# Optimization experiments

Hardware: AMD Instinct MI355X
Metric: run time of the kernel (lower is better)

Reference implementation:

```python
import jax, jax.numpy as jnp
import numpy as np

NUM_NODES = 10000  # fixed by input spec: edge_index values in [0, 10000)


def setup_inputs() -> dict:
    key = jax.random.key(0)
    k1, k2, k3 = jax.random.split(key, 3)
    N, E, D_IN, D_OUT = NUM_NODES, 320000, 256, 256
    x = jax.random.normal(k1, (N, D_IN), dtype=jnp.float32)
    edge_index = jax.random.randint(k2, (2, E), 0, N, dtype=jnp.int64)
    # ensure node N-1 appears so num_nodes == N as in the torch code
    edge_index = edge_index.at[0, 0].set(N - 1)
    # xavier_uniform for [D_IN, D_OUT]
    limit = float(np.sqrt(6.0 / (D_IN + D_OUT)))
    weight = jax.random.uniform(k3, (D_IN, D_OUT), dtype=jnp.float32,
                                minval=-limit, maxval=limit)
    return {"x": x, "edge_index": edge_index, "weight": weight}


def _normalize_adjacency(edge_index, num_nodes):
    src, dst = edge_index[0], edge_index[1]
    ones = jnp.ones(src.shape[0], dtype=jnp.float32)
    # symmetric binarized adjacency: adj[i,j] = adj[j,i] = 1 (set, not add)
    adj = jnp.zeros((num_nodes, num_nodes), dtype=jnp.float32)
    adj = adj.at[src, dst].max(ones)
    adj = adj.at[dst, src].max(ones)
    # one round of self-loops: adj += I
    adj = adj + jnp.eye(num_nodes, dtype=jnp.float32)
    deg = jnp.sum(adj, axis=1)                    # [N]
    dinv = 1.0 / jnp.sqrt(deg)                    # [N]
    # D^-1/2 A D^-1/2 via broadcasting (equivalent to diag mms)
    return adj * dinv[:, None] * dinv[None, :]


def reference(x, edge_index, weight):
    adj = _normalize_adjacency(edge_index, NUM_NODES)  # [N, N]
    h = adj @ x                                        # [N, D_IN]
    return h @ weight                                  # [N, D_OUT]
```

## Files before the change

kernel.cpp:

```cpp
#include <hip/hip_runtime.h>
#include <hip/hip_bf16.h>
#include <stdint.h>

#define N_NODES   10000
#define D_FEAT    256
#define E_EDGES   320000
#define ROW_WORDS 313
#define ROW_STRIDE 320
#define LIST_CAP  1024

#define NB    250
#define RPB   40
#define B_CAP 8192

typedef __attribute__((ext_vector_type(4))) float float4v;
typedef _Float16 half8  __attribute__((ext_vector_type(8)));
typedef _Float16 half4v __attribute__((ext_vector_type(4)));

__device__ __forceinline__ uint16_t f2bf(float f) {
    union { float f; uint32_t u; } v; v.f = f;
    uint32_t r = v.u + 0x7fffu + ((v.u >> 16) & 1u);
    return (uint16_t)(r >> 16);
}
__device__ __forceinline__ float lo16(uint32_t u) {
    union { uint32_t u; float f; } v; v.u = u << 16; return v.f;
}
__device__ __forceinline__ float hi16(uint32_t u) {
    union { uint32_t u; float f; } v; v.u = u & 0xffff0000u; return v.f;
}


__global__ void __launch_bounds__(1024)
fill_buckets(const int* __restrict__ ei, uint32_t* __restrict__ bucketbuf,
             uint32_t* __restrict__ cursors) {
    __shared__ uint32_t hist[NB];
    __shared__ uint32_t base_s[NB];
    int t = threadIdx.x;
    for (int b = t; b < NB; b += 1024) hist[b] = 0;
    __syncthreads();
    int e = blockIdx.x * 1024 + t;
    int b0 = -1, b1 = -1; uint32_t ent0 = 0, ent1 = 0, slot0 = 0, slot1 = 0;
    if (e < E_EDGES) {
        int s = ei[e], d = ei[E_EDGES + e];
        if ((uint32_t)s < N_NODES && (uint32_t)d < N_NODES) {
            b0 = s / RPB; ent0 = ((uint32_t)(s - b0 * RPB) << 14) | (uint32_t)d;
            b1 = d / RPB; ent1 = ((uint32_t)(d - b1 * RPB) << 14) | (uint32_t)s;
            slot0 = atomicAdd(&hist[b0], 1u);
            slot1 = atomicAdd(&hist[b1], 1u);
        }
    }
    __syncthreads();
    for (int b = t; b < NB; b += 1024)
        base_s[b] = hist[b] ? atomicAdd(&cursors[b], hist[b]) : 0u;
    __syncthreads();
    if (b0 >= 0) {
        uint32_t p0 = base_s[b0] + slot0;
        if (p0 < B_CAP) bucketbuf[(size_t)b0 * B_CAP + p0] = ent0;
        uint32_t p1 = base_s[b1] + slot1;
        if (p1 < B_CAP) bucketbuf[(size_t)b1 * B_CAP + p1] = ent1;
    }
}

__global__ void __launch_bounds__(1024)
bucket_to_csr(const uint32_t* __restrict__ bucketbuf,
              const uint32_t* __restrict__ cursors,
              uint32_t* __restrict__ gcursor,
              uint32_t* __restrict__ col, uint32_t* __restrict__ row_base,
              uint32_t* __restrict__ row_deg, float* __restrict__ dinv) {
    __shared__ uint32_t bm[RPB * ROW_WORDS];
    __shared__ uint32_t degs[RPB];
    __shared__ uint32_t rowoff[RPB];
    __shared__ uint32_t segbase;
    int b = blockIdx.x, t = threadIdx.x;
    for (int i = t; i < RPB * ROW_WORDS; i += 1024) bm[i] = 0;
    __syncthreads();
    uint32_t cnt = min(cursors[b], (uint32_t)B_CAP);
    const uint32_t* bb = bucketbuf + (size_t)b * B_CAP;
    for (uint32_t i = t; i < cnt; i += 1024) {
        uint32_t ent = bb[i];
        uint32_t lr = ent >> 14, d = ent & 0x3FFFu;
        atomicOr(&bm[lr * ROW_WORDS + (d >> 5)], 1u << (d & 31));
    }
    __syncthreads();
    int wv = t >> 6, lane = t & 63;
    for (int r = wv; r < RPB; r += 16) {
        int pop = 0;
        #pragma unroll
        for (int k = 0; k < 5; k++) {
            int w = lane + 64 * k;
            if (w < ROW_WORDS) pop += __popc(bm[r * ROW_WORDS + w]);
        }
        #pragma unroll
        for (int off = 32; off > 0; off >>= 1) pop += __shfl_xor(pop, off, 64);
        if (lane == 0) degs[r] = (uint32_t)pop;
    }
    __syncthreads();
    if (t == 0) {
        uint32_t run = 0;
        for (int r = 0; r < RPB; r++) {
            rowoff[r] = run;
            run += (degs[r] + 3u) & ~3u;
        }
        segbase = atomicAdd(gcursor, run);
    }
    __syncthreads();
    int row0 = b * RPB;
    for (int r = wv; r < RPB; r += 16) {
        int gi = row0 + r;
        uint32_t base = segbase + rowoff[r];
        if (lane == 0) {
            row_base[gi] = base;
            row_deg[gi]  = degs[r];
            dinv[gi]     = 1.0f / sqrtf((float)(degs[r] + 1u));
        }
        uint32_t wb[5]; int tot = 0;
        #pragma unroll
        for (int k = 0; k < 5; k++) {
            int w = lane + 64 * k;
            uint32_t v = (w < ROW_WORDS) ? bm[r * ROW_WORDS + w] : 0u;
            wb[k] = v; tot += __popc(v);
        }
        int incl = tot;
        #pragma unroll
        for (int off = 1; off < 64; off <<= 1) {
            int v = __shfl_up(incl, off, 64);
            if (lane >= off) incl += v;
        }
        uint32_t p = base + (uint32_t)(incl - tot);
        #pragma unroll
        for (int k = 0; k < 5; k++) {
            uint32_t bits = wb[k];
            uint32_t cbase = (uint32_t)(lane + 64 * k) << 5;
            while (bits) {
                col[p++] = cbase + (uint32_t)__builtin_ctz(bits);
                bits &= bits - 1;
            }
        }
    }
}

__global__ void __launch_bounds__(256)
scale_cast(const float* __restrict__ dinv, const float* __restrict__ x,
           uint16_t* __restrict__ xs) {
    int wv = threadIdx.x >> 6, lane = threadIdx.x & 63;
    int i = blockIdx.x * 4 + wv;
    float di = dinv[i];
    float4v v = *(const float4v*)(x + (size_t)i * D_FEAT + lane * 4);
    uint2 o;
    o.x = (uint32_t)f2bf(di * v[0]) | ((uint32_t)f2bf(di * v[1]) << 16);
    o.y = (uint32_t)f2bf(di * v[2]) | ((uint32_t)f2bf(di * v[3]) << 16);
    *(uint2*)(xs + (size_t)i * D_FEAT + lane * 4) = o;
}

__global__ void __launch_bounds__(256)
wcast(const float* __restrict__ w, _Float16* __restrict__ wt) {
    int k = blockIdx.x, n = threadIdx.x;
    wt[(size_t)n * D_FEAT + k] = (_Float16)w[(size_t)k * D_FEAT + n];
}

__global__ void __launch_bounds__(256)
spmm_csr(const uint32_t* __restrict__ row_base, const uint32_t* __restrict__ row_deg,
         const float* __restrict__ dinv, const uint32_t* __restrict__ col,
         const uint16_t* __restrict__ xs, _Float16* __restrict__ aggh) {
    int wv = threadIdx.x >> 6, lane = threadIdx.x & 63;
    int i = blockIdx.x * 4 + wv;
    uint32_t base = row_base[i], deg = row_deg[i];
    float di = dinv[i];
    float4v z = {0.f, 0.f, 0.f, 0.f};
    float4v acc0 = z, acc1 = z, acc2 = z, acc3 = z;
    size_t ch = (size_t)lane * 4;
    uint32_t t4 = deg & ~3u;
    for (uint32_t t = 0; t < t4; t += 4) {
        uint4 jv = *(const uint4*)&col[base + t];
        uint2 g0 = *(const uint2*)(xs + (size_t)jv.x * D_FEAT + ch);
        uint2 g1 = *(const uint2*)(xs + (size_t)jv.y * D_FEAT + ch);
        uint2 g2 = *(const uint2*)(xs + (size_t)jv.z * D_FEAT + ch);
        uint2 g3 = *(const uint2*)(xs + (size_t)jv.w * D_FEAT + ch);
        acc0[0] += lo16(g0.x); acc0[1] += hi16(g0.x); acc0[2] += lo16(g0.y); acc0[3] += hi16(g0.y);
        acc1[0] += lo16(g1.x); acc1[1] += hi16(g1.x); acc1[2] += lo16(g1.y); acc1[3] += hi16(g1.y);
        acc2[0] += lo16(g2.x); acc2[1] += hi16(g2.x); acc2[2] += lo16(g2.y); acc2[3] += hi16(g2.y);
        acc3[0] += lo16(g3.x); acc3[1] += hi16(g3.x); acc3[2] += lo16(g3.y); acc3[3] += hi16(g3.y);
    }
    for (uint32_t t = t4; t < deg; t++) {
        uint32_t j = col[base + t];
        uint2 g = *(const uint2*)(xs + (size_t)j * D_FEAT + ch);
        acc0[0] += lo16(g.x); acc0[1] += hi16(g.x); acc0[2] += lo16(g.y); acc0[3] += hi16(g.y);
    }
    uint2 gs = *(const uint2*)(xs + (size_t)i * D_FEAT + ch);
    acc1[0] += lo16(gs.x); acc1[1] += hi16(gs.x); acc1[2] += lo16(gs.y); acc1[3] += hi16(gs.y);
    float4v acc = (acc0 + acc1) + (acc2 + acc3);
    half4v o = { (_Float16)(di * acc[0]), (_Float16)(di * acc[1]),
                 (_Float16)(di * acc[2]), (_Float16)(di * acc[3]) };
    *(half4v*)(aggh + (size_t)i * D_FEAT + ch) = o;
}

__global__ void __launch_bounds__(256)
gemm_mfma(const _Float16* __restrict__ aggh, const _Float16* __restrict__ wt,
          float* __restrict__ out) {
    int t = threadIdx.x;
    int wv = t >> 6, lane = t & 63;
    int quad = lane >> 4, r = lane & 15;
    int bx = blockIdx.x;
    int ct = blockIdx.y * 4 + wv;

    const _Float16* pa = aggh + (size_t)(bx * 16 + r) * D_FEAT + quad * 8;
    const _Float16* pb = wt   + (size_t)(ct * 16 + r) * D_FEAT + quad * 8;

    float4v acc = {0.f, 0.f, 0.f, 0.f};
    #pragma unroll
    for (int kk = 0; kk < D_FEAT; kk += 32) {
        half8 a = *(const half8*)(pa + kk);
        half8 b = *(const half8*)(pb + kk);
        acc = __builtin_amdgcn_mfma_f32_16x16x32_f16(a, b, acc, 0, 0, 0);
    }
    int mbase = bx * 16 + quad * 4;
    int colg  = ct * 16 + r;
    #pragma unroll
    for (int u = 0; u < 4; u++)
        out[(size_t)(mbase + u) * D_FEAT + colg] = acc[u];
}


__global__ void scatter_edges_fb(const int* __restrict__ ei,
                                 uint32_t* __restrict__ bitmap) {
    int e = blockIdx.x * blockDim.x + threadIdx.x;
    if (e >= E_EDGES) return;
    int s = ei[e], d = ei[E_EDGES + e];
    if ((uint32_t)s >= N_NODES || (uint32_t)d >= N_NODES) return;
    atomicOr(&bitmap[(size_t)s * ROW_STRIDE + (d >> 5)], 1u << (d & 31));
    atomicOr(&bitmap[(size_t)d * ROW_STRIDE + (s >> 5)], 1u << (s & 31));
}

__global__ void __launch_bounds__(256)
popc_dinv(const uint32_t* __restrict__ bitmap, float* __restrict__ dinv) {
    int wv = threadIdx.x >> 6, lane = threadIdx.x & 63;
    int i = blockIdx.x * 4 + wv;
    const uint32_t* rb = bitmap + (size_t)i * ROW_STRIDE;
    int pop = 0;
    #pragma unroll
    for (int k = 0; k < 5; k++) {
        int w = lane + 64 * k;
        if (w < ROW_WORDS) pop += __popc(rb[w]);
    }
    #pragma unroll
    for (int off = 32; off > 0; off >>= 1) pop += __shfl_xor(pop, off, 64);
    if (lane == 0) dinv[i] = 1.0f / sqrtf((float)(pop + 1));
}

__global__ void __launch_bounds__(256)
spmm_bitmap_fb(const uint32_t* __restrict__ bitmap, const float* __restrict__ dinv,
               const float* __restrict__ xf, float* __restrict__ agg) {
    __shared__ __align__(16) uint32_t lists[4][LIST_CAP];
    int wv = threadIdx.x >> 6, lane = threadIdx.x & 63;
    int i = blockIdx.x * 4 + wv;
    uint32_t* list = lists[wv];
    const uint32_t* rb = bitmap + (size_t)i * ROW_STRIDE;

    uint32_t wbits[5]; int tot = 0;
    #pragma unroll
    for (int k = 0; k < 5; k++) {
        int w = lane + 64 * k;
        uint32_t b = (w < ROW_WORDS) ? rb[w] : 0u;
        wbits[k] = b;
        tot += __popc(b);
    }
    int incl = tot;
    #pragma unroll
    for (int off = 1; off < 64; off <<= 1) {
        int v = __shfl_up(incl, off, 64);
        if (lane >= off) incl += v;
    }
    uint32_t p = (uint32_t)(incl - tot);
    uint32_t deg = (uint32_t)__shfl(incl, 63, 64);
    #pragma unroll
    for (int k = 0; k < 5; k++) {
        uint32_t bits = wbits[k];
        uint32_t base = (uint32_t)(lane + 64 * k) << 5;
        while (bits) {
            if (p < LIST_CAP) list[p] = base + (uint32_t)__builtin_ctz(bits);
            p++;
            bits &= bits - 1;
        }
    }
    if (deg > LIST_CAP) deg = LIST_CAP;

    float di = dinv[i];
    float4v z = {0.f, 0.f, 0.f, 0.f};
    float4v acc0 = z, acc1 = z, acc2 = z, acc3 = z;
    float4v sv = *(const float4v*)(xf + (size_t)i * D_FEAT + lane * 4);
    uint32_t t4 = deg & ~3u;
    for (uint32_t t = 0; t < t4; t += 4) {
        uint4 jv = *(const uint4*)&list[t];
        float d0 = dinv[jv.x], d1 = dinv[jv.y], d2 = dinv[jv.z], d3 = dinv[jv.w];
        float4v v0 = *(const float4v*)(xf + (size_t)jv.x * D_FEAT + lane * 4);
        float4v v1 = *(const float4v*)(xf + (size_t)jv.y * D_FEAT + lane * 4);
        float4v v2 = *(const float4v*)(xf + (size_t)jv.z * D_FEAT + lane * 4);
        float4v v3 = *(const float4v*)(xf + (size_t)jv.w * D_FEAT + lane * 4);
        acc0 += d0 * v0; acc1 += d1 * v1; acc2 += d2 * v2; acc3 += d3 * v3;
    }
    for (uint32_t t = t4; t < deg; t++) {
        uint32_t j = list[t];
        acc0 += dinv[j] * (*(const float4v*)(xf + (size_t)j * D_FEAT + lane * 4));
    }
    float4v acc = (acc0 + acc1) + (acc2 + acc3) + di * sv;
    *(float4v*)(agg + (size_t)i * D_FEAT + lane * 4) = di * acc;
}

__global__ void __launch_bounds__(256)
gemm_valu(float* __restrict__ io, const float* __restrict__ wf) {
    __shared__ __align__(16) float a_lds[16 * D_FEAT];
    int c = threadIdx.x;
    int r0 = blockIdx.x * 16;
    for (int idx = c; idx < 16 * D_FEAT; idx += 256)
        a_lds[idx] = io[(size_t)r0 * D_FEAT + idx];
    __syncthreads();
    float acc[16];
    #pragma unroll
    for (int r = 0; r < 16; r++) acc[r] = 0.f;
    for (int k0 = 0; k0 < D_FEAT; k0 += 4) {
        float w0 = wf[(size_t)(k0 + 0) * D_FEAT + c];
        float w1 = wf[(size_t)(k0 + 1) * D_FEAT + c];
        float w2 = wf[(size_t)(k0 + 2) * D_FEAT + c];
        float w3 = wf[(size_t)(k0 + 3) * D_FEAT + c];
        #pragma unroll
        for (int r = 0; r < 16; r++) {
            float4v av = *(const float4v*)&a_lds[r * D_FEAT + k0];
            acc[r] = fmaf(av[3], w3, fmaf(av[2], w2,
                     fmaf(av[1], w1, fmaf(av[0], w0, acc[r]))));
        }
    }
    #pragma unroll
    for (int r = 0; r < 16; r++)
        io[(size_t)(r0 + r) * D_FEAT + c] = acc[r];
}

extern "C" void kernel_launch(void* const* d_in, const int* in_sizes, int n_in,
                              void* d_out, int out_size, void* d_ws, size_t ws_size,
                              hipStream_t stream) {
    const float* x  = (const float*)d_in[0];
    const int*   ei = (const int*)d_in[1];
    const float* w  = (const float*)d_in[2];
    float* out = (float*)d_out;
    uint8_t* ws = (uint8_t*)d_ws;

    const size_t CUR_OFF  = 8192000;
    const size_t RB_OFF   = 8194048;
    const size_t RD_OFF   = 8234048;
    const size_t DI_OFF   = 8274048;
    const size_t XS_OFF   = 8314048;
    const size_t COL_OFF  = 13434048;
    const size_t WT_OFF   = 16154048;
    const size_t NEED_NEW = 16285120;
    const size_t NEED_FB  = 12840000;

    if (ws_size >= NEED_NEW) {
        uint32_t* bucketbuf = (uint32_t*)ws;
        _Float16* aggh      = (_Float16*)ws;
        uint32_t* cursors   = (uint32_t*)(ws + CUR_OFF);
        uint32_t* row_base  = (uint32_t*)(ws + RB_OFF);
        uint32_t* row_deg   = (uint32_t*)(ws + RD_OFF);
        float*    dinv      = (float*)(ws + DI_OFF);
        uint16_t* xs        = (uint16_t*)(ws + XS_OFF);
        uint32_t* col       = (uint32_t*)(ws + COL_OFF);
        _Float16* wt        = (_Float16*)(ws + WT_OFF);

        hipMemsetAsync(cursors, 0, 2048, stream);
        fill_buckets <<<(E_EDGES + 1023) / 1024, 1024, 0, stream>>>(ei, bucketbuf, cursors);
        bucket_to_csr<<<NB, 1024, 0, stream>>>(bucketbuf, cursors, &cursors[NB],
                                               col, row_base, row_deg, dinv);
        wcast        <<<D_FEAT, D_FEAT, 0, stream>>>(w, wt);
        scale_cast   <<<N_NODES / 4, 256, 0, stream>>>(dinv, x, xs);
        spmm_csr     <<<N_NODES / 4, 256, 0, stream>>>(row_base, row_deg, dinv, col, xs, aggh);
        gemm_mfma    <<<dim3(N_NODES / 16, 4), 256, 0, stream>>>(aggh, wt, out);
    } else if (ws_size >= NEED_FB) {
        uint32_t* bitmap = (uint32_t*)ws;
        float*    dinv   = (float*)(ws + 12800000);

        hipMemsetAsync(bitmap, 0, 12800000, stream);
        scatter_edges_fb<<<(E_EDGES + 255) / 256, 256, 0, stream>>>(ei, bitmap);
        popc_dinv      <<<N_NODES / 4, 256, 0, stream>>>(bitmap, dinv);
        spmm_bitmap_fb <<<N_NODES / 4, 256, 0, stream>>>(bitmap, dinv, x, out);
        gemm_valu      <<<N_NODES / 16, 256, 0, stream>>>(out, w);
    }
}
```

Baseline: 147.5 us.

## Fuse SpMM with MFMA GEMM via LDS and stage bucket writes in fill_buckets

Merges the sparse aggregation and the dense weight GEMM into one kernel. Each block aggregates 16 rows into LDS as fp16, then runs MFMA over all 256 output columns, so the intermediate aggregate never goes through global memory and one launch is removed. Separately, fill_buckets now does a local prefix scan and stages entries sorted by bucket in LDS, so the global bucket writes are more contiguous. The cost is fewer blocks for the SpMM (2500 down to 625), each doing 4 rows per wave, which lowers parallelism and latency hiding for the gather.

```diff
diff --git a/kernel.cpp b/kernel.cpp
--- a/kernel.cpp
+++ b/kernel.cpp
@@ -13,6 +13,8 @@
 #define RPB   40
 #define B_CAP 8192
 
+#define LDSTR 264
+
 typedef __attribute__((ext_vector_type(4))) float float4v;
 typedef _Float16 half8  __attribute__((ext_vector_type(8)));
 typedef _Float16 half4v __attribute__((ext_vector_type(4)));
@@ -33,31 +35,48 @@
 __global__ void __launch_bounds__(1024)
 fill_buckets(const int* __restrict__ ei, uint32_t* __restrict__ bucketbuf,
              uint32_t* __restrict__ cursors) {
-    __shared__ uint32_t hist[NB];
-    __shared__ uint32_t base_s[NB];
+    __shared__ uint32_t hist[256];
+    __shared__ uint32_t lofs[256];
+    __shared__ uint32_t base_s[256];
+    __shared__ uint32_t stage[2048];
+    __shared__ uint16_t sbkt[2048];
     int t = threadIdx.x;
-    for (int b = t; b < NB; b += 1024) hist[b] = 0;
+    if (t < 256) hist[t] = 0;
     __syncthreads();
     int e = blockIdx.x * 1024 + t;
-    int b0 = -1, b1 = -1; uint32_t ent0 = 0, ent1 = 0, slot0 = 0, slot1 = 0;
+    int b0 = -1, b1 = -1; uint32_t ent0 = 0, ent1 = 0, s0 = 0, s1 = 0;
     if (e < E_EDGES) {
         int s = ei[e], d = ei[E_EDGES + e];
         if ((uint32_t)s < N_NODES && (uint32_t)d < N_NODES) {
             b0 = s / RPB; ent0 = ((uint32_t)(s - b0 * RPB) << 14) | (uint32_t)d;
             b1 = d / RPB; ent1 = ((uint32_t)(d - b1 * RPB) << 14) | (uint32_t)s;
-            slot0 = atomicAdd(&hist[b0], 1u);
-            slot1 = atomicAdd(&hist[b1], 1u);
-        }
-    }
-    __syncthreads();
-    for (int b = t; b < NB; b += 1024)
-        base_s[b] = hist[b] ? atomicAdd(&cursors[b], hist[b]) : 0u;
-    __syncthreads();
+            s0 = atomicAdd(&hist[b0], 1u);
+            s1 = atomicAdd(&hist[b1], 1u);
+        }
+    }
+    __syncthreads();
+    if (t < 256) lofs[t] = hist[t];
+    __syncthreads();
+    for (int d = 1; d < 256; d <<= 1) {
+        uint32_t v = 0;
+        if (t < 256 && t >= d) v = lofs[t - d];
+        __syncthreads();
+        if (t < 256) lofs[t] += v;
+        __syncthreads();
+    }
+    if (t < 256) base_s[t] = hist[t] ? atomicAdd(&cursors[t], hist[t]) : 0u;
     if (b0 >= 0) {
-        uint32_t p0 = base_s[b0] + slot0;
-        if (p0 < B_CAP) bucketbuf[(size_t)b0 * B_CAP + p0] = ent0;
-        uint32_t p1 = base_s[b1] + slot1;
-        if (p1 < B_CAP) bucketbuf[(size_t)b1 * B_CAP + p1] = ent1;
+        uint32_t p0 = lofs[b0] - hist[b0] + s0;
+        stage[p0] = ent0; sbkt[p0] = (uint16_t)b0;
+        uint32_t p1 = lofs[b1] - hist[b1] + s1;
+        stage[p1] = ent1; sbkt[p1] = (uint16_t)b1;
+    }
+    __syncthreads();
+    uint32_t total = lofs[255];
+    for (uint32_t idx = t; idx < total; idx += 1024) {
+        uint32_t b = sbkt[idx];
+        uint32_t pos = base_s[b] + (idx - (lofs[b] - hist[b]));
+        if (pos < B_CAP) bucketbuf[(size_t)b * B_CAP + pos] = stage[idx];
     }
 }
 
@@ -159,65 +178,65 @@
 }
 
 __global__ void __launch_bounds__(256)
-spmm_csr(const uint32_t* __restrict__ row_base, const uint32_t* __restrict__ row_deg,
-         const float* __restrict__ dinv, const uint32_t* __restrict__ col,
-         const uint16_t* __restrict__ xs, _Float16* __restrict__ aggh) {
-    int wv = threadIdx.x >> 6, lane = threadIdx.x & 63;
-    int i = blockIdx.x * 4 + wv;
-    uint32_t base = row_base[i], deg = row_deg[i];
-    float di = dinv[i];
-    float4v z = {0.f, 0.f, 0.f, 0.f};
-    float4v acc0 = z, acc1 = z, acc2 = z, acc3 = z;
+spmm_gemm(const uint32_t* __restrict__ row_base, const uint32_t* __restrict__ row_deg,
+          const float* __restrict__ dinv, const uint32_t* __restrict__ col,
+          const uint16_t* __restrict__ xs, const _Float16* __restrict__ wt,
+          float* __restrict__ out) {
+    __shared__ __align__(16) _Float16 a_lds[16 * LDSTR];
+    int t = threadIdx.x, wv = t >> 6, lane = t & 63;
+    int r0 = blockIdx.x * 16;
     size_t ch = (size_t)lane * 4;
-    uint32_t t4 = deg & ~3u;
-    for (uint32_t t = 0; t < t4; t += 4) {
-        uint4 jv = *(const uint4*)&col[base + t];
-        uint2 g0 = *(const uint2*)(xs + (size_t)jv.x * D_FEAT + ch);
-        uint2 g1 = *(const uint2*)(xs + (size_t)jv.y * D_FEAT + ch);
-        uint2 g2 = *(const uint2*)(xs + (size_t)jv.z * D_FEAT + ch);
-        uint2 g3 = *(const uint2*)(xs + (size_t)jv.w * D_FEAT + ch);
-        acc0[0] += lo16(g0.x); acc0[1] += hi16(g0.x); acc0[2] += lo16(g0.y); acc0[3] += hi16(g0.y);
-        acc1[0] += lo16(g1.x); acc1[1] += hi16(g1.x); acc1[2] += lo16(g1.y); acc1[3] += hi16(g1.y);
-        acc2[0] += lo16(g2.x); acc2[1] += hi16(g2.x); acc2[2] += lo16(g2.y); acc2[3] += hi16(g2.y);
-        acc3[0] += lo16(g3.x); acc3[1] += hi16(g3.x); acc3[2] += lo16(g3.y); acc3[3] += hi16(g3.y);
-    }
-    for (uint32_t t = t4; t < deg; t++) {
-        uint32_t j = col[base + t];
-        uint2 g = *(const uint2*)(xs + (size_t)j * D_FEAT + ch);
-        acc0[0] += lo16(g.x); acc0[1] += hi16(g.x); acc0[2] += lo16(g.y); acc0[3] += hi16(g.y);
-    }
-    uint2 gs = *(const uint2*)(xs + (size_t)i * D_FEAT + ch);
-    acc1[0] += lo16(gs.x); acc1[1] += hi16(gs.x); acc1[2] += lo16(gs.y); acc1[3] += hi16(gs.y);
-    float4v acc = (acc0 + acc1) + (acc2 + acc3);
-    half4v o = { (_Float16)(di * acc[0]), (_Float16)(di * acc[1]),
-                 (_Float16)(di * acc[2]), (_Float16)(di * acc[3]) };
-    *(half4v*)(aggh + (size_t)i * D_FEAT + ch) = o;
-}
-
-__global__ void __launch_bounds__(256)
-gemm_mfma(const _Float16* __restrict__ aggh, const _Float16* __restrict__ wt,
-          float* __restrict__ out) {
-    int t = threadIdx.x;
-    int wv = t >> 6, lane = t & 63;
+
+    for (int rr = wv; rr < 16; rr += 4) {
+        int i = r0 + rr;
+        uint32_t base = row_base[i], deg = row_deg[i];
+        float di = dinv[i];
+        float4v z = {0.f, 0.f, 0.f, 0.f};
+        float4v acc0 = z, acc1 = z, acc2 = z, acc3 = z;
+        uint32_t t4 = deg & ~3u;
+        for (uint32_t k = 0; k < t4; k += 4) {
+            uint4 jv = *(const uint4*)&col[base + k];
+            uint2 g0 = *(const uint2*)(xs + (size_t)jv.x * D_FEAT + ch);
+            uint2 g1 = *(const uint2*)(xs + (size_t)jv.y * D_FEAT + ch);
+            uint2 g2 = *(const uint2*)(xs + (size_t)jv.z * D_FEAT + ch);
+            uint2 g3 = *(const uint2*)(xs + (size_t)jv.w * D_FEAT + ch);
+            acc0[0] += lo16(g0.x); acc0[1] += hi16(g0.x); acc0[2] += lo16(g0.y); acc0[3] += hi16(g0.y);
+            acc1[0] += lo16(g1.x); acc1[1] += hi16(g1.x); acc1[2] += lo16(g1.y); acc1[3] += hi16(g1.y);
+            acc2[0] += lo16(g2.x); acc2[1] += hi16(g2.x); acc2[2] += lo16(g2.y); acc2[3] += hi16(g2.y);
+            acc3[0] += lo16(g3.x); acc3[1] += hi16(g3.x); acc3[2] += lo16(g3.y); acc3[3] += hi16(g3.y);
+        }
+        for (uint32_t k = t4; k < deg; k++) {
+            uint32_t j = col[base + k];
+            uint2 g = *(const uint2*)(xs + (size_t)j * D_FEAT + ch);
+            acc0[0] += lo16(g.x); acc0[1] += hi16(g.x); acc0[2] += lo16(g.y); acc0[3] += hi16(g.y);
+        }
+        uint2 gs = *(const uint2*)(xs + (size_t)i * D_FEAT + ch);
+        acc1[0] += lo16(gs.x); acc1[1] += hi16(gs.x); acc1[2] += lo16(gs.y); acc1[3] += hi16(gs.y);
+        float4v acc = (acc0 + acc1) + (acc2 + acc3);
+        half4v o = { (_Float16)(di * acc[0]), (_Float16)(di * acc[1]),
+                     (_Float16)(di * acc[2]), (_Float16)(di * acc[3]) };
+        *(half4v*)&a_lds[rr * LDSTR + lane * 4] = o;
+    }
+    __syncthreads();
+
     int quad = lane >> 4, r = lane & 15;
-    int bx = blockIdx.x;
-    int ct = blockIdx.y * 4 + wv;
-
-    const _Float16* pa = aggh + (size_t)(bx * 16 + r) * D_FEAT + quad * 8;
-    const _Float16* pb = wt   + (size_t)(ct * 16 + r) * D_FEAT + quad * 8;
-
-    float4v acc = {0.f, 0.f, 0.f, 0.f};
-    #pragma unroll
-    for (int kk = 0; kk < D_FEAT; kk += 32) {
-        half8 a = *(const half8*)(pa + kk);
-        half8 b = *(const half8*)(pb + kk);
-        acc = __builtin_amdgcn_mfma_f32_16x16x32_f16(a, b, acc, 0, 0, 0);
-    }
-    int mbase = bx * 16 + quad * 4;
-    int colg  = ct * 16 + r;
-    #pragma unroll
-    for (int u = 0; u < 4; u++)
-        out[(size_t)(mbase + u) * D_FEAT + colg] = acc[u];
+    int mbase = r0 + quad * 4;
+    #pragma unroll
+    for (int u = 0; u < 4; u++) {
+        int ct = wv * 4 + u;
+        const _Float16* pb = wt + (size_t)(ct * 16 + r) * D_FEAT + quad * 8;
+        float4v acc = {0.f, 0.f, 0.f, 0.f};
+        #pragma unroll
+        for (int kk = 0; kk < D_FEAT; kk += 32) {
+            half8 a = *(const half8*)&a_lds[r * LDSTR + kk + quad * 8];
+            half8 b = *(const half8*)(pb + kk);
+            acc = __builtin_amdgcn_mfma_f32_16x16x32_f16(a, b, acc, 0, 0, 0);
+        }
+        int colg = ct * 16 + r;
+        #pragma unroll
+        for (int v = 0; v < 4; v++)
+            out[(size_t)(mbase + v) * D_FEAT + colg] = acc[v];
+    }
 }
 
 
@@ -289,8 +308,8 @@
     float4v acc0 = z, acc1 = z, acc2 = z, acc3 = z;
     float4v sv = *(const float4v*)(xf + (size_t)i * D_FEAT + lane * 4);
     uint32_t t4 = deg & ~3u;
-    for (uint32_t t = 0; t < t4; t += 4) {
-        uint4 jv = *(const uint4*)&list[t];
+    for (uint32_t k = 0; k < t4; k += 4) {
+        uint4 jv = *(const uint4*)&list[k];
         float d0 = dinv[jv.x], d1 = dinv[jv.y], d2 = dinv[jv.z], d3 = dinv[jv.w];
         float4v v0 = *(const float4v*)(xf + (size_t)jv.x * D_FEAT + lane * 4);
         float4v v1 = *(const float4v*)(xf + (size_t)jv.y * D_FEAT + lane * 4);
@@ -298,8 +317,8 @@
         float4v v3 = *(const float4v*)(xf + (size_t)jv.w * D_FEAT + lane * 4);
         acc0 += d0 * v0; acc1 += d1 * v1; acc2 += d2 * v2; acc3 += d3 * v3;
     }
-    for (uint32_t t = t4; t < deg; t++) {
-        uint32_t j = list[t];
+    for (uint32_t k = t4; k < deg; k++) {
+        uint32_t j = list[k];
         acc0 += dinv[j] * (*(const float4v*)(xf + (size_t)j * D_FEAT + lane * 4));
     }
     float4v acc = (acc0 + acc1) + (acc2 + acc3) + di * sv;
@@ -355,7 +374,6 @@
 
     if (ws_size >= NEED_NEW) {
         uint32_t* bucketbuf = (uint32_t*)ws;
-        _Float16* aggh      = (_Float16*)ws;
         uint32_t* cursors   = (uint32_t*)(ws + CUR_OFF);
         uint32_t* row_base  = (uint32_t*)(ws + RB_OFF);
         uint32_t* row_deg   = (uint32_t*)(ws + RD_OFF);
@@ -370,8 +388,8 @@
                                                col, row_base, row_deg, dinv);
         wcast        <<<D_FEAT, D_FEAT, 0, stream>>>(w, wt);
         scale_cast   <<<N_NODES / 4, 256, 0, stream>>>(dinv, x, xs);
-        spmm_csr     <<<N_NODES / 4, 256, 0, stream>>>(row_base, row_deg, dinv, col, xs, aggh);
-        gemm_mfma    <<<dim3(N_NODES / 16, 4), 256, 0, stream>>>(aggh, wt, out);
+        spmm_gemm    <<<N_NODES / 16, 256, 0, stream>>>(row_base, row_deg, dinv,
+                                                        col, xs, wt, out);
     } else if (ws_size >= NEED_FB) {
         uint32_t* bitmap = (uint32_t*)ws;
         float*    dinv   = (float*)(ws + 12800000);
```

Measured after the change: 158.4 us. 1.07x slower.
